# Kernel tuning notes

Hardware: AMD Instinct MI355X
Metric: run time of the kernel (lower is better)

Reference implementation:

```python
import jax, jax.numpy as jnp
import numpy as np

MEM_LEN = 2048      # memory_len
N_TURNS = 8         # user-facing n_turns (module stores N_TURNS+1)
RATE = 2            # compression_rate
B, S, D = 32, 512, 1024
N_CONV = sum(RATE ** i for i in range(1, N_TURNS + 1))  # 510


def setup_inputs() -> dict:
    key = jax.random.key(0)
    k1, k2, k3 = jax.random.split(key, 3)
    inputs = jax.random.normal(k1, (B, S, D), dtype=jnp.float32)
    memory = jax.random.normal(k2, (MEM_LEN + N_CONV, D), dtype=jnp.float32)
    filters = jax.random.normal(k3, (RATE, D, D), dtype=jnp.float32) * (1.0 / np.sqrt(RATE * D))
    return {"inputs": inputs, "memory": memory, "filters": filters}


def _compress(x, filters):
    # x: (L, D) -> (L // RATE, D): strided VALID conv1d, filter (width=RATE, in=D, out=D)
    y = jax.lax.conv_general_dilated(
        x[None], filters, window_strides=(RATE,), padding='VALID',
        dimension_numbers=('NWC', 'WIO', 'NWC'))
    return y[0]


def _memory_pass(x, memory, filters):
    # x: (S, D); replicates HelixMemory._memory_pass for one batch element.
    new_memory = jnp.concatenate([memory, x], axis=0)        # (MEM_LEN+N_CONV+S, D)
    short = new_memory[-MEM_LEN:]                            # (MEM_LEN, D)
    long_mem = new_memory[:-MEM_LEN][:-S]                    # (N_CONV, D)
    fallout = short[-S:]                                     # (S, D) == x (S<=MEM_LEN)
    helix = jnp.concatenate([long_mem, _compress(fallout, filters)], axis=0)  # (N_CONV+S//RATE, D)
    new_mem = short
    # stored n_turns = N_TURNS+1; loop k = 1..N_TURNS (unrolled, all shapes static)
    for k in range(1, N_TURNS + 1):
        n_long = sum(RATE ** i for i in range(1, N_TURNS + 2 - k))
        turn = RATE ** (N_TURNS + 1 - k)
        add = helix.shape[0] - n_long                         # > 0 for all k here
        old = helix[-turn - add:-add]                         # (turn, D)
        part = helix[-turn:]                                  # (turn, D)
        helix = jnp.concatenate([helix[:-turn - add], _compress(old, filters)], axis=0)
        new_mem = jnp.concatenate([part, new_mem], axis=0)
    return new_mem                                            # (MEM_LEN+N_CONV, D)


def reference(inputs, memory, filters):
    # (B, S, D) -> (B, MEM_LEN+N_CONV, D)
    return jax.vmap(lambda x: _memory_pass(x, memory, filters))(inputs)
```

## Files before the change

kernel.cpp:

```cpp
#include <hip/hip_runtime.h>
#include <hip/hip_bf16.h>

#define B_SZ 32
#define S_SZ 512
#define D_SZ 1024
#define MEM_ROWS 2558
#define OUT_ROW_STRIDE 2558
#define K_DIM 2048
#define M_BATCH 8192
#define M_TOTAL 8448
#define N_DIM 1024

typedef _Float16 half8 __attribute__((ext_vector_type(8)));
typedef _Float16 half4v __attribute__((ext_vector_type(4)));
typedef float f32x4 __attribute__((ext_vector_type(4)));

#define LDS_STRIDE 40

__global__ __launch_bounds__(256) void transpose_w(const float* __restrict__ f,
                                                   _Float16* __restrict__ wt) {
    __shared__ float tile[32][33];
    const int k0 = blockIdx.x * 32;
    const int n0 = blockIdx.y * 32;
    const int tx = threadIdx.x;
    const int ty = threadIdx.y;
#pragma unroll
    for (int i = 0; i < 32; i += 8)
        tile[ty + i][tx] = f[(size_t)(k0 + ty + i) * 1024 + n0 + tx];
    __syncthreads();
#pragma unroll
    for (int i = 0; i < 32; i += 8)
        wt[(size_t)(n0 + ty + i) * 2048 + k0 + tx] = (_Float16)tile[tx][ty + i];
}

__global__ __launch_bounds__(256) void gemm_kernel(const float* __restrict__ inputs,
                                                   const float* __restrict__ memory,
                                                   const _Float16* __restrict__ wt,
                                                   float* __restrict__ out,
                                                   float* __restrict__ ws_c) {
    __shared__ _Float16 a_lds[128 * LDS_STRIDE];
    __shared__ _Float16 b_lds[128 * LDS_STRIDE];

    const int tid = threadIdx.x;
    const int bm = blockIdx.x;
    const int bn = blockIdx.y;
    const int m_base = bm * 128;
    const int n_base = bn * 128;

    const int wave = tid >> 6;
    const int lane = tid & 63;
    const int q = lane >> 4;
    const int lm = lane & 15;
    const int wm = (wave >> 1) * 64;
    const int wn = (wave & 1) * 64;

    f32x4 acc[4][4] = {};

    const float* a_src[4];
#pragma unroll
    for (int it = 0; it < 4; ++it) {
        int pos = it * 256 + tid;
        int row = pos >> 3;
        int m = m_base + row;
        const float* p = nullptr;
        if (m < M_BATCH) {
            p = inputs + (size_t)(m >> 8) * (S_SZ * D_SZ) + (size_t)(m & 255) * 2048;
        } else {
            int r = m - M_BATCH;
            if (r < 254) p = memory + (size_t)(2 * r + 2) * 1024;
        }
        a_src[it] = p;
    }

    for (int kt = 0; kt < K_DIM / 32; ++kt) {
        const int k0 = kt * 32;
        __syncthreads();
#pragma unroll
        for (int it = 0; it < 4; ++it) {
            int pos = it * 256 + tid;
            int row = pos >> 3, c4 = pos & 7;
            float4 v = {0.f, 0.f, 0.f, 0.f};
            if (a_src[it]) v = *(const float4*)(a_src[it] + k0 + c4 * 4);
            half4v h;
            h[0] = (_Float16)v.x; h[1] = (_Float16)v.y;
            h[2] = (_Float16)v.z; h[3] = (_Float16)v.w;
            *(half4v*)(&a_lds[row * LDS_STRIDE + c4 * 4]) = h;
        }
#pragma unroll
        for (int it = 0; it < 2; ++it) {
            int pos = it * 256 + tid;
            int row = pos >> 2, c8 = pos & 3;
            uint4 v = *(const uint4*)(wt + (size_t)(n_base + row) * 2048 + k0 + c8 * 8);
            *(uint4*)(&b_lds[row * LDS_STRIDE + c8 * 8]) = v;
        }
        __syncthreads();

        half8 a_frag[4], b_frag[4];
#pragma unroll
        for (int t = 0; t < 4; ++t) {
            a_frag[t] = *(const half8*)(&a_lds[(wm + t * 16 + lm) * LDS_STRIDE + q * 8]);
            b_frag[t] = *(const half8*)(&b_lds[(wn + t * 16 + lm) * LDS_STRIDE + q * 8]);
        }
#pragma unroll
        for (int i = 0; i < 4; ++i)
#pragma unroll
            for (int j = 0; j < 4; ++j)
                acc[i][j] = __builtin_amdgcn_mfma_f32_16x16x32_f16(a_frag[i], b_frag[j],
                                                                   acc[i][j], 0, 0, 0);
    }

#pragma unroll
    for (int i = 0; i < 4; ++i) {
        const int m0 = m_base + wm + i * 16 + q * 4;
#pragma unroll
        for (int j = 0; j < 4; ++j) {
            const int n = n_base + wn + j * 16 + lm;
#pragma unroll
            for (int rg = 0; rg < 4; ++rg) {
                const int m = m0 + rg;
                const float v = acc[i][j][rg];
                if (m < M_BATCH) {
                    const int b = m >> 8;
                    const int row = 254 + (m & 255);
                    out[(size_t)b * (OUT_ROW_STRIDE * D_SZ) + (size_t)row * 1024 + n] = v;
                } else {
                    const int r = m - M_BATCH;
                    if (r < 254) ws_c[(size_t)r * 1024 + n] = v;
                }
            }
        }
    }
}

__global__ __launch_bounds__(256) void assemble_kernel(const float* __restrict__ inputs,
                                                       const float* __restrict__ memory,
                                                       const float* __restrict__ ws_c,
                                                       float* __restrict__ out) {
    const int b = blockIdx.y;
    const int r = blockIdx.x;
    const int col = threadIdx.x * 4;
    float4 v;
    size_t dst_row;
    if (r < 254) {
        v = *(const float4*)(ws_c + (size_t)r * 1024 + col);
        dst_row = r;
    } else if (r < 1790) {
        v = *(const float4*)(memory + (size_t)(1022 + r - 254) * 1024 + col);
        dst_row = 510 + (r - 254);
    } else {
        v = *(const float4*)(inputs + (size_t)b * (S_SZ * D_SZ) + (size_t)(r - 1790) * 1024 + col);
        dst_row = 2046 + (r - 1790);
    }
    *(float4*)(out + (size_t)b * (OUT_ROW_STRIDE * D_SZ) + dst_row * 1024 + col) = v;
}

extern "C" void kernel_launch(void* const* d_in, const int* in_sizes, int n_in,
                              void* d_out, int out_size, void* d_ws, size_t ws_size,
                              hipStream_t stream) {
    const float* inputs  = (const float*)d_in[0];
    const float* memory  = (const float*)d_in[1];
    const float* filters = (const float*)d_in[2];
    float* out = (float*)d_out;

    _Float16* wt = (_Float16*)d_ws;
    float* ws_c  = (float*)((char*)d_ws + 4 * 1024 * 1024);

    transpose_w<<<dim3(64, 32), dim3(32, 8), 0, stream>>>(filters, wt);
    gemm_kernel<<<dim3(66, 8), 256, 0, stream>>>(inputs, memory, wt, out, ws_c);
    assemble_kernel<<<dim3(2302, 32), 256, 0, stream>>>(inputs, memory, ws_c, out);
}
```

Measured before the change: 575.8 us.

## Pre-convert A to fp16 and load GEMM tiles via async global-to-LDS copies

New measurement: 519.2 us. 1.11x faster.

```diff
diff --git a/kernel.cpp b/kernel.cpp
--- a/kernel.cpp
+++ b/kernel.cpp
@@ -4,7 +4,6 @@
 #define B_SZ 32
 #define S_SZ 512
 #define D_SZ 1024
-#define MEM_ROWS 2558
 #define OUT_ROW_STRIDE 2558
 #define K_DIM 2048
 #define M_BATCH 8192
@@ -15,7 +14,11 @@
 typedef _Float16 half4v __attribute__((ext_vector_type(4)));
 typedef float f32x4 __attribute__((ext_vector_type(4)));
 
-#define LDS_STRIDE 40
+__device__ __forceinline__ void async_copy16(const void* g, void* l) {
+    __builtin_amdgcn_global_load_lds(
+        (const __attribute__((address_space(1))) unsigned int*)g,
+        (__attribute__((address_space(3))) unsigned int*)l, 16, 0, 0);
+}
 
 __global__ __launch_bounds__(256) void transpose_w(const float* __restrict__ f,
                                                    _Float16* __restrict__ wt) {
@@ -33,19 +36,43 @@
         wt[(size_t)(n0 + ty + i) * 2048 + k0 + tx] = (_Float16)tile[tx][ty + i];
 }
 
-__global__ __launch_bounds__(256) void gemm_kernel(const float* __restrict__ inputs,
-                                                   const float* __restrict__ memory,
-                                                   const _Float16* __restrict__ wt,
-                                                   float* __restrict__ out,
-                                                   float* __restrict__ ws_c) {
-    __shared__ _Float16 a_lds[128 * LDS_STRIDE];
-    __shared__ _Float16 b_lds[128 * LDS_STRIDE];
+__global__ __launch_bounds__(256) void convert_a(const float* __restrict__ inputs,
+                                                 const float* __restrict__ memory,
+                                                 _Float16* __restrict__ a16) {
+    const int m = blockIdx.x;
+    const int c = threadIdx.x * 8;
+    const float* src = nullptr;
+    if (m < M_BATCH) {
+        src = inputs + (size_t)m * 2048;
+    } else {
+        int r = m - M_BATCH;
+        if (r < 254) src = memory + (size_t)(2 * r + 2) * 1024;
+    }
+    half8 h;
+    if (src) {
+        float4 v0 = *(const float4*)(src + c);
+        float4 v1 = *(const float4*)(src + c + 4);
+        h[0] = (_Float16)v0.x; h[1] = (_Float16)v0.y;
+        h[2] = (_Float16)v0.z; h[3] = (_Float16)v0.w;
+        h[4] = (_Float16)v1.x; h[5] = (_Float16)v1.y;
+        h[6] = (_Float16)v1.z; h[7] = (_Float16)v1.w;
+    } else {
+#pragma unroll
+        for (int i = 0; i < 8; ++i) h[i] = (_Float16)0.f;
+    }
+    *(half8*)(a16 + (size_t)m * 2048 + c) = h;
+}
+
+__global__ __launch_bounds__(256) void gemm_async(const _Float16* __restrict__ a16,
+                                                  const _Float16* __restrict__ wt,
+                                                  float* __restrict__ out,
+                                                  float* __restrict__ ws_c) {
+    __shared__ _Float16 a_lds[128 * 32];
+    __shared__ _Float16 b_lds[128 * 32];
 
     const int tid = threadIdx.x;
-    const int bm = blockIdx.x;
-    const int bn = blockIdx.y;
-    const int m_base = bm * 128;
-    const int n_base = bn * 128;
+    const int m_base = blockIdx.x * 128;
+    const int n_base = blockIdx.y * 128;
 
     const int wave = tid >> 6;
     const int lane = tid & 63;
@@ -54,8 +81,80 @@
     const int wm = (wave >> 1) * 64;
     const int wn = (wave & 1) * 64;
 
+    const int srow = wave * 16 + (lane >> 2);
+    const int kc = (lane & 3) * 8;
+    const _Float16* ag0 = a16 + (size_t)(m_base + srow) * 2048 + kc;
+    const _Float16* ag1 = a16 + (size_t)(m_base + 64 + srow) * 2048 + kc;
+    const _Float16* bg0 = wt + (size_t)(n_base + srow) * 2048 + kc;
+    const _Float16* bg1 = wt + (size_t)(n_base + 64 + srow) * 2048 + kc;
+    _Float16* al0 = a_lds + wave * 512;
+    _Float16* al1 = a_lds + 2048 + wave * 512;
+    _Float16* bl0 = b_lds + wave * 512;
+    _Float16* bl1 = b_lds + 2048 + wave * 512;
+
     f32x4 acc[4][4] = {};
 
+    for (int kt = 0; kt < K_DIM / 32; ++kt) {
+        const int k0 = kt * 32;
+        __syncthreads();
+        async_copy16(ag0 + k0, al0);
+        async_copy16(ag1 + k0, al1);
+        async_copy16(bg0 + k0, bl0);
+        async_copy16(bg1 + k0, bl1);
+        __syncthreads();
+
+        half8 a_frag[4], b_frag[4];
+#pragma unroll
+        for (int t = 0; t < 4; ++t) {
+            a_frag[t] = *(const half8*)(&a_lds[(wm + t * 16 + lm) * 32 + q * 8]);
+            b_frag[t] = *(const half8*)(&b_lds[(wn + t * 16 + lm) * 32 + q * 8]);
+        }
+#pragma unroll
+        for (int i = 0; i < 4; ++i)
+#pragma unroll
+            for (int j = 0; j < 4; ++j)
+                acc[i][j] = __builtin_amdgcn_mfma_f32_16x16x32_f16(a_frag[i], b_frag[j],
+                                                                   acc[i][j], 0, 0, 0);
+    }
+
+#pragma unroll
+    for (int i = 0; i < 4; ++i) {
+        const int m0 = m_base + wm + i * 16 + q * 4;
+#pragma unroll
+        for (int j = 0; j < 4; ++j) {
+            const int n = n_base + wn + j * 16 + lm;
+#pragma unroll
+            for (int rg = 0; rg < 4; ++rg) {
+                const int m = m0 + rg;
+                const float v = acc[i][j][rg];
+                if (m < M_BATCH) {
+                    const int b = m >> 8;
+                    const int row = 254 + (m & 255);
+                    out[(size_t)b * (OUT_ROW_STRIDE * D_SZ) + (size_t)row * 1024 + n] = v;
+                } else {
+                    const int r = m - M_BATCH;
+                    if (r < 254) ws_c[(size_t)r * 1024 + n] = v;
+                }
+            }
+        }
+    }
+}
+
+#define LDS_STRIDE 40
+__global__ __launch_bounds__(256) void gemm_fallback(const float* __restrict__ inputs,
+                                                     const float* __restrict__ memory,
+                                                     const _Float16* __restrict__ wt,
+                                                     float* __restrict__ out,
+                                                     float* __restrict__ ws_c) {
+    __shared__ _Float16 a_lds[128 * LDS_STRIDE];
+    __shared__ _Float16 b_lds[128 * LDS_STRIDE];
+    const int tid = threadIdx.x;
+    const int m_base = blockIdx.x * 128;
+    const int n_base = blockIdx.y * 128;
+    const int wave = tid >> 6, lane = tid & 63;
+    const int q = lane >> 4, lm = lane & 15;
+    const int wm = (wave >> 1) * 64, wn = (wave & 1) * 64;
+    f32x4 acc[4][4] = {};
     const float* a_src[4];
 #pragma unroll
     for (int it = 0; it < 4; ++it) {
@@ -63,15 +162,10 @@
         int row = pos >> 3;
         int m = m_base + row;
         const float* p = nullptr;
-        if (m < M_BATCH) {
-            p = inputs + (size_t)(m >> 8) * (S_SZ * D_SZ) + (size_t)(m & 255) * 2048;
-        } else {
-            int r = m - M_BATCH;
-            if (r < 254) p = memory + (size_t)(2 * r + 2) * 1024;
-        }
+        if (m < M_BATCH) p = inputs + (size_t)m * 2048;
+        else { int r = m - M_BATCH; if (r < 254) p = memory + (size_t)(2 * r + 2) * 1024; }
         a_src[it] = p;
     }
-
     for (int kt = 0; kt < K_DIM / 32; ++kt) {
         const int k0 = kt * 32;
         __syncthreads();
@@ -94,7 +188,6 @@
             *(uint4*)(&b_lds[row * LDS_STRIDE + c8 * 8]) = v;
         }
         __syncthreads();
-
         half8 a_frag[4], b_frag[4];
 #pragma unroll
         for (int t = 0; t < 4; ++t) {
@@ -108,7 +201,6 @@
                 acc[i][j] = __builtin_amdgcn_mfma_f32_16x16x32_f16(a_frag[i], b_frag[j],
                                                                    acc[i][j], 0, 0, 0);
     }
-
 #pragma unroll
     for (int i = 0; i < 4; ++i) {
         const int m0 = m_base + wm + i * 16 + q * 4;
@@ -162,10 +254,22 @@
     const float* filters = (const float*)d_in[2];
     float* out = (float*)d_out;
 
+    const size_t WT_BYTES  = (size_t)N_DIM * K_DIM * 2;
+    const size_t A16_BYTES = (size_t)M_TOTAL * K_DIM * 2;
+    const size_t NEED = WT_BYTES + A16_BYTES + (size_t)254 * 1024 * 4;
+
     _Float16* wt = (_Float16*)d_ws;
-    float* ws_c  = (float*)((char*)d_ws + 4 * 1024 * 1024);
-
     transpose_w<<<dim3(64, 32), dim3(32, 8), 0, stream>>>(filters, wt);
-    gemm_kernel<<<dim3(66, 8), 256, 0, stream>>>(inputs, memory, wt, out, ws_c);
-    assemble_kernel<<<dim3(2302, 32), 256, 0, stream>>>(inputs, memory, ws_c, out);
-}
+
+    if (ws_size >= NEED) {
+        _Float16* a16 = (_Float16*)((char*)d_ws + WT_BYTES);
+        float* ws_c   = (float*)((char*)d_ws + WT_BYTES + A16_BYTES);
+        convert_a<<<dim3(M_TOTAL), 256, 0, stream>>>(inputs, memory, a16);
+        gemm_async<<<dim3(66, 8), 256, 0, stream>>>(a16, wt, out, ws_c);
+        assemble_kernel<<<dim3(2302, 32), 256, 0, stream>>>(inputs, memory, ws_c, out);
+    } else {
+        float* ws_c = (float*)((char*)d_ws + WT_BYTES);
+        gemm_fallback<<<dim3(66, 8), 256, 0, stream>>>(inputs, memory, wt, out, ws_c);
+        assemble_kernel<<<dim3(2302, 32), 256, 0, stream>>>(inputs, memory, ws_c, out);
+    }
+}
```
